# Kernel optimization log

Measured on AMD Instinct MI355X. Metric: run time of the kernel, lower is better.

The kernel has to match this reference:

```python
import jax, jax.numpy as jnp
import numpy as np

B, P, S, FX, FY, D, DFF = 8, 1, 2048, 16, 16, 512, 2048


def _ln(x, g, b, eps=1e-6):
    m = jnp.mean(x, axis=-1, keepdims=True)
    v = jnp.var(x, axis=-1, keepdims=True)
    return g * (x - m) / jnp.sqrt(v + eps) + b


def setup_inputs() -> dict:
    key = jax.random.key(0)
    ks = jax.random.split(key, 16)
    sc = 0.02
    inp = {
        'inputs': jax.random.normal(ks[0], (B, P, S, FX), dtype=jnp.float32),
        'targets': jax.random.normal(ks[1], (B, P, S, FY), dtype=jnp.float32),
        # input projection Dense(d_model)
        'Wp': jax.random.normal(ks[2], (FX, D), dtype=jnp.float32) * sc,
        'bp': jnp.zeros((D,), jnp.float32),
        # attention projections wq/wk/wv/dense (all Dense(d_model))
        'Wq': jax.random.normal(ks[3], (D, D), dtype=jnp.float32) * sc,
        'bq': jnp.zeros((D,), jnp.float32),
        'Wk': jax.random.normal(ks[4], (D, D), dtype=jnp.float32) * sc,
        'bk': jnp.zeros((D,), jnp.float32),
        'Wv': jax.random.normal(ks[5], (D, D), dtype=jnp.float32) * sc,
        'bv': jnp.zeros((D,), jnp.float32),
        'Wo': jax.random.normal(ks[6], (D, D), dtype=jnp.float32) * sc,
        'bo': jnp.zeros((D,), jnp.float32),
        # layernorm 1 / 2
        'g1': jnp.ones((D,), jnp.float32),
        'beta1': jnp.zeros((D,), jnp.float32),
        'g2': jnp.ones((D,), jnp.float32),
        'beta2': jnp.zeros((D,), jnp.float32),
        # pointwise FFN Dense(dff, relu) -> Dense(d_model)
        'Wf1': jax.random.normal(ks[7], (D, DFF), dtype=jnp.float32) * sc,
        'bf1': jnp.zeros((DFF,), jnp.float32),
        'Wf2': jax.random.normal(ks[8], (DFF, D), dtype=jnp.float32) * sc,
        'bf2': jnp.zeros((D,), jnp.float32),
        # final output layer Dense(output_size)
        'Wfin': jax.random.normal(ks[9], (D, FY), dtype=jnp.float32) * sc,
        'bfin': jnp.zeros((FY,), jnp.float32),
    }
    return inp


def reference(inputs, targets, Wp, bp, Wq, bq, Wk, bk, Wv, bv, Wo, bo,
              g1, beta1, g2, beta2, Wf1, bf1, Wf2, bf2, Wfin, bfin):
    d = jnp.float32(Wp.shape[1])
    # projection_layer_ts then *sqrt(d_model)
    x = (inputs @ Wp + bp) * jnp.sqrt(d)                      # (B,P,S,D)
    q = x @ Wq + bq
    k = x @ Wk + bk
    v = x @ Wv + bv
    # with noise=False and no resampling, the per-step SMC recurrence equals
    # causal self-attention (at step t, K/V hold rows <= t, rest are zero-masked)
    logits = jnp.einsum('bpqd,bpkd->bpqk', q, k) / jnp.sqrt(d)  # (B,P,S,S)
    Sdim = x.shape[2]
    causal = jnp.tril(jnp.ones((Sdim, Sdim), dtype=bool))
    logits = jnp.where(causal, logits, jnp.float32(-1e9))
    attn = jax.nn.softmax(logits, axis=-1)                    # attention weights per step
    z = jnp.einsum('bpqk,bpkd->bpqd', attn, v)
    z = z @ Wo + bo
    # full_model: LN(z+x) -> FFN -> LN(ffn+out)
    out = _ln(z + x, g1, beta1)
    ff = jax.nn.relu(out @ Wf1 + bf1) @ Wf2 + bf2
    r = _ln(ff + out, g2, beta2)                              # R trajectory (B,P,S,D)
    pred = r @ Wfin + bfin                                    # (B,P,S,F_y)
    # no resampling (noise=False): R_resampl == R, pred_resampl == pred
    return (pred, pred, k, v, r, attn)
```

## Files before the change

### kernel.cpp

```cpp
#include <hip/hip_runtime.h>
#include <hip/hip_bf16.h>
#include <stdint.h>

#define BB 8
#define SS 2048
#define TT (BB*SS)
#define DD 512
#define DFFX 2048

static __device__ const float SQRTD  = 22.627416997969522f;
static __device__ const float INVSQD = 0.04419417382415922f;

typedef __attribute__((ext_vector_type(4))) float  f32x4_t;
typedef __attribute__((ext_vector_type(8))) __bf16 bf16x8_t;
typedef __attribute__((ext_vector_type(4))) __bf16 bf16x4_t;
typedef __attribute__((ext_vector_type(2))) __bf16 bf16x2_t;

static __device__ __forceinline__ bf16x8_t mk_frag(bf16x4_t lo, bf16x4_t hi) {
  return __builtin_shufflevector(lo, hi, 0, 1, 2, 3, 4, 5, 6, 7);
}

typedef __attribute__((address_space(1))) const unsigned int g_u32;
typedef __attribute__((address_space(3))) unsigned int lds_u32;
static __device__ __forceinline__ void gld16(const void* g, void* l) {
  __builtin_amdgcn_global_load_lds((g_u32*)g, (lds_u32*)l, 16, 0, 0);
}

__global__ __launch_bounds__(256) void transpose_conv3(
    const float* __restrict__ Wo, const float* __restrict__ Wf1,
    const float* __restrict__ Wf2, __bf16* __restrict__ Wo_t,
    __bf16* __restrict__ Wf1_t, __bf16* __restrict__ Wf2_t) {
  const int bx = blockIdx.x;
  const float* src; __bf16* dst; int C, R, gx, gy;
  if (bx < 256)       { src = Wo;  dst = Wo_t;  R = 512;  C = 512;  gx = bx & 15;  gy = bx >> 4; }
  else if (bx < 1280) { const int b = bx - 256;  src = Wf1; dst = Wf1_t; R = 512;  C = 2048; gx = b & 63; gy = b >> 6; }
  else                { const int b = bx - 1280; src = Wf2; dst = Wf2_t; R = 2048; C = 512;  gx = b & 15; gy = b >> 4; }
  __shared__ float tile[32][33];
  const int c0 = gx * 32, r0 = gy * 32;
  const int tx = threadIdx.x & 31, ty = threadIdx.x >> 5;
#pragma unroll
  for (int i = 0; i < 4; i++)
    tile[ty + 8*i][tx] = src[(size_t)(r0 + ty + 8*i) * C + c0 + tx];
  __syncthreads();
#pragma unroll
  for (int i = 0; i < 4; i++)
    dst[(size_t)(c0 + ty + 8*i) * R + r0 + tx] = (__bf16)tile[tx][ty + 8*i];
}

__global__ __launch_bounds__(256) void fold_kernel(
    const float* __restrict__ Wp, const float* __restrict__ bp,
    const float* __restrict__ Wq, const float* __restrict__ bq,
    const float* __restrict__ Wk, const float* __restrict__ bk,
    const float* __restrict__ Wv, const float* __restrict__ bv,
    float* __restrict__ Wfold, float* __restrict__ bfold) {
  __shared__ float wp[16][512];
  __shared__ float bps[512];
  for (int i = threadIdx.x; i < 16 * 512; i += 256) wp[i >> 9][i & 511] = Wp[i];
  for (int i = threadIdx.x; i < 512; i += 256) bps[i] = bp[i];
  __syncthreads();
  const int cl = threadIdx.x & 15, r = threadIdx.x >> 4;
  const int cg = blockIdx.x * 16 + cl;
  const int sub = cg >> 9, wc = cg & 511;
  const float* W = sub == 0 ? Wq : sub == 1 ? Wk : Wv;
  const float* bb = sub == 0 ? bq : sub == 1 ? bk : bv;
  float acc = 0.f, bacc = 0.f;
  for (int k = 0; k < 512; k += 4) {
    const float4 wpv = *(const float4*)&wp[r][k];
    const float g0 = W[(size_t)k * 512 + wc];
    const float g1 = W[(size_t)(k + 1) * 512 + wc];
    const float g2 = W[(size_t)(k + 2) * 512 + wc];
    const float g3 = W[(size_t)(k + 3) * 512 + wc];
    acc += wpv.x * g0 + wpv.y * g1 + wpv.z * g2 + wpv.w * g3;
    if (r == 0) {
      const float4 b4 = *(const float4*)&bps[k];
      bacc += b4.x * g0 + b4.y * g1 + b4.z * g2 + b4.w * g3;
    }
  }
  Wfold[(size_t)r * 1536 + cg] = acc * SQRTD;
  if (r == 0) bfold[cg] = bacc * SQRTD + bb[wc];
}

__global__ __launch_bounds__(256) void smallk_kernel(
    const float* __restrict__ inp,
    const float* __restrict__ Wfold, const float* __restrict__ bfold,
    const float* __restrict__ Wp, const float* __restrict__ bp,
    __bf16* __restrict__ qb, __bf16* __restrict__ kb, __bf16* __restrict__ vb,
    __bf16* __restrict__ xb, float* __restrict__ o_k, float* __restrict__ o_v) {
  const int sl = blockIdx.y;
  const float* W; const float* bias; int ldw; float scale;
  __bf16* ob; float* fo;
  if (sl == 3) { W = Wp; bias = bp; ldw = 512; scale = SQRTD; ob = xb; fo = nullptr; }
  else {
    W = Wfold + sl * 512; bias = bfold + sl * 512; ldw = 1536; scale = 1.f;
    ob = sl == 0 ? qb : sl == 1 ? kb : vb;
    fo = sl == 0 ? (float*)nullptr : sl == 1 ? o_k : o_v;
  }
  __shared__ float ivl[16][16];
  const int tid = threadIdx.x;
  ivl[tid >> 4][tid & 15] = inp[(size_t)blockIdx.x * 256 + tid];
  const int c0 = 2 * tid;
  float w0[16], w1[16];
#pragma unroll
  for (int r = 0; r < 16; r++) {
    w0[r] = W[(size_t)r * ldw + c0];
    w1[r] = W[(size_t)r * ldw + c0 + 1];
  }
  const float bb0 = bias[c0], bb1 = bias[c0 + 1];
  __syncthreads();
#pragma unroll 4
  for (int tt = 0; tt < 16; ++tt) {
    const float4 i0 = *(const float4*)&ivl[tt][0];
    const float4 i1 = *(const float4*)&ivl[tt][4];
    const float4 i2 = *(const float4*)&ivl[tt][8];
    const float4 i3 = *(const float4*)&ivl[tt][12];
    float a0, a1;
    a0  = i0.x * w0[0];   a1  = i0.x * w1[0];
    a0 += i0.y * w0[1];   a1 += i0.y * w1[1];
    a0 += i0.z * w0[2];   a1 += i0.z * w1[2];
    a0 += i0.w * w0[3];   a1 += i0.w * w1[3];
    a0 += i1.x * w0[4];   a1 += i1.x * w1[4];
    a0 += i1.y * w0[5];   a1 += i1.y * w1[5];
    a0 += i1.z * w0[6];   a1 += i1.z * w1[6];
    a0 += i1.w * w0[7];   a1 += i1.w * w1[7];
    a0 += i2.x * w0[8];   a1 += i2.x * w1[8];
    a0 += i2.y * w0[9];   a1 += i2.y * w1[9];
    a0 += i2.z * w0[10];  a1 += i2.z * w1[10];
    a0 += i2.w * w0[11];  a1 += i2.w * w1[11];
    a0 += i3.x * w0[12];  a1 += i3.x * w1[12];
    a0 += i3.y * w0[13];  a1 += i3.y * w1[13];
    a0 += i3.z * w0[14];  a1 += i3.z * w1[14];
    a0 += i3.w * w0[15];  a1 += i3.w * w1[15];
    const float v0 = (a0 + bb0) * scale;
    const float v1 = (a1 + bb1) * scale;
    const size_t t = (size_t)blockIdx.x * 16 + tt;
    bf16x2_t pv; pv[0] = (__bf16)v0; pv[1] = (__bf16)v1;
    *(bf16x2_t*)(ob + t * 512 + c0) = pv;
    if (fo) {
      float2 fv; fv.x = v0; fv.y = v1;
      *(float2*)(fo + t * 512 + c0) = fv;
    }
  }
}

__global__ __launch_bounds__(256) void attn_prep_kernel(
    const __bf16* __restrict__ qbuf, const __bf16* __restrict__ kbuf,
    const __bf16* __restrict__ vbuf, const __bf16* __restrict__ Wo_t,
    __bf16* __restrict__ pb, __bf16* __restrict__ vwt) {
  const int bx = blockIdx.x, by = blockIdx.y;
  const int z = blockIdx.z;
  const int m0 = by * 128;
  const bool isScore = bx < 16;
  const int n0 = (isScore ? bx : bx - 16) * 128;
  if (isScore && n0 > m0 + 127) return;
  const __bf16* A  = (isScore ? qbuf : vbuf) + (size_t)z * SS * DD;
  const __bf16* Bt = isScore ? (kbuf + (size_t)z * SS * DD) : Wo_t;
  constexpr int K = DD;

  __shared__ __align__(16) __bf16 As[3 * 128 * 32];
  __shared__ __align__(16) __bf16 Bs[3 * 128 * 32];
  const int tid = threadIdx.x, lane = tid & 63, wave = tid >> 6;
  const int l15 = lane & 15, g = lane >> 4;
  const int wr = wave >> 1, wc = wave & 1;

  const int srow0 = wave * 32 + (lane >> 2);
  const int srow1 = srow0 + 16;
  const int sc0 = (((lane & 3) ^ ((srow0 >> 1) & 3)) << 4);
  const int sc1 = (((lane & 3) ^ ((srow1 >> 1) & 3)) << 4);
  const char* ga0 = (const char*)(A + (size_t)(m0 + srow0) * K) + sc0;
  const char* ga1 = (const char*)(A + (size_t)(m0 + srow1) * K) + sc1;
  const char* gb0 = (const char*)(Bt + (size_t)(n0 + srow0) * K) + sc0;
  const char* gb1 = (const char*)(Bt + (size_t)(n0 + srow1) * K) + sc1;

  const int plo = (g >> 1) ^ ((l15 >> 1) & 3);
  const int aof0 = (wr * 64 + l15) * 64 + plo * 16 + (g & 1) * 8;
  const int bof0 = (wc * 64 + l15) * 64 + plo * 16 + (g & 1) * 8;

  f32x4_t acc[4][4];
#pragma unroll
  for (int i = 0; i < 4; i++)
#pragma unroll
    for (int j = 0; j < 4; j++) acc[i][j] = (f32x4_t){0.f, 0.f, 0.f, 0.f};

  auto STAGE = [&](const int buf, const int k0) {
    const size_t kb = (size_t)k0 * 2;
    char* la = (char*)As + buf * 8192 + wave * 2048;
    char* lb = (char*)Bs + buf * 8192 + wave * 2048;
    gld16(ga0 + kb, la);
    gld16(ga1 + kb, la + 1024);
    gld16(gb0 + kb, lb);
    gld16(gb1 + kb, lb + 1024);
  };
  auto COMPUTE = [&](const int buf) {
    const char* AsB = (const char*)As + buf * 8192;
    const char* BsB = (const char*)Bs + buf * 8192;
    bf16x8_t af[4], bfr[4];
#pragma unroll
    for (int i = 0; i < 4; i++) {
      const int ao = aof0 + i * 1024;
      af[i] = mk_frag(*(const bf16x4_t*)(AsB + ao),
                      *(const bf16x4_t*)(AsB + (ao ^ 32)));
      const int bo = bof0 + i * 1024;
      bfr[i] = mk_frag(*(const bf16x4_t*)(BsB + bo),
                       *(const bf16x4_t*)(BsB + (bo ^ 32)));
    }
#pragma unroll
    for (int i = 0; i < 4; i++)
#pragma unroll
      for (int j = 0; j < 4; j++)
        acc[i][j] = __builtin_amdgcn_mfma_f32_16x16x32_bf16(af[i], bfr[j], acc[i][j], 0, 0, 0);
  };

  const int nt = K >> 5;
  STAGE(0, 0);
  STAGE(1, 32);
  STAGE(2, 64);
  int cur = 0;
  for (int t = 0; t < nt; ++t) {
    const int rem = nt - 1 - t;
    if (rem >= 2)      asm volatile("s_waitcnt vmcnt(8)" ::: "memory");
    else if (rem == 1) asm volatile("s_waitcnt vmcnt(4)" ::: "memory");
    else               asm volatile("s_waitcnt vmcnt(0)" ::: "memory");
    __builtin_amdgcn_s_barrier();
    COMPUTE(cur);
    __builtin_amdgcn_s_barrier();
    if (t + 3 < nt) STAGE(cur, (t + 3) << 5);
    cur = (cur == 2) ? 0 : cur + 1;
  }

#pragma unroll
  for (int i = 0; i < 4; i++) {
#pragma unroll
    for (int j = 0; j < 4; j++) {
      const int col = n0 + wc * 64 + j * 16 + l15;
      if (isScore) {
#pragma unroll
        for (int r = 0; r < 4; r++) {
          const int row = m0 + wr * 64 + i * 16 + g * 4 + r;
          pb[(size_t)z * SS * SS + (size_t)row * SS + col] =
              (__bf16)(acc[i][j][r] * INVSQD);
        }
      } else {
        const int row0 = m0 + wr * 64 + i * 16 + g * 4;
        bf16x4_t tv;
#pragma unroll
        for (int r = 0; r < 4; r++) tv[r] = (__bf16)acc[i][j][r];
        *(bf16x4_t*)(vwt + (size_t)z * SS * DD + (size_t)col * SS + row0) = tv;
      }
    }
  }
}

template <bool CAUSAL, bool RELU, bool RES, bool XCDS>
__global__ __launch_bounds__(256) void gemm128(
    const __bf16* __restrict__ A, const __bf16* __restrict__ Bt,
    const float* __restrict__ bias, const __bf16* __restrict__ Res,
    __bf16* __restrict__ Cb,
    int N, int K, size_t aBatch, size_t bBatch, size_t cBatch) {
  int bx = blockIdx.x, by = blockIdx.y;
  if (XCDS) {
    const int nwg = (int)(gridDim.x * gridDim.y);
    const int cpx = nwg >> 3;
    const int lin = (int)(blockIdx.y * gridDim.x + blockIdx.x);
    const int nl = (lin & 7) * cpx + (lin >> 3);
    by = nl / (int)gridDim.x;
    bx = nl - by * (int)gridDim.x;
  }
  const int n0 = bx * 128;
  const int m0 = by * 128;
  __shared__ __align__(16) __bf16 As[3 * 128 * 32];
  __shared__ __align__(16) __bf16 Bs[3 * 128 * 32];
  const int tid = threadIdx.x, lane = tid & 63, wave = tid >> 6;
  const int l15 = lane & 15, g = lane >> 4;
  const int wr = wave >> 1, wc = wave & 1;

  const int srow0 = wave * 32 + (lane >> 2);
  const int srow1 = srow0 + 16;
  const int sc0 = (((lane & 3) ^ ((srow0 >> 1) & 3)) << 4);
  const int sc1 = (((lane & 3) ^ ((srow1 >> 1) & 3)) << 4);
  const size_t aOff = (size_t)blockIdx.z * aBatch;
  const size_t bOff = (size_t)blockIdx.z * bBatch;
  const size_t cOff = (size_t)blockIdx.z * cBatch;
  const char* gb0 = (const char*)(Bt + bOff + (size_t)(n0 + srow0) * K) + sc0;
  const char* gb1 = (const char*)(Bt + bOff + (size_t)(n0 + srow1) * K) + sc1;
  const char* ga0 = (const char*)(A + aOff + (size_t)(m0 + srow0) * K) + sc0;
  const char* ga1 = (const char*)(A + aOff + (size_t)(m0 + srow1) * K) + sc1;

  const int plo = (g >> 1) ^ ((l15 >> 1) & 3);
  const int aof0 = (wr * 64 + l15) * 64 + plo * 16 + (g & 1) * 8;
  const int bof0 = (wc * 64 + l15) * 64 + plo * 16 + (g & 1) * 8;

  f32x4_t acc[4][4];
#pragma unroll
  for (int i = 0; i < 4; i++)
#pragma unroll
    for (int j = 0; j < 4; j++) acc[i][j] = (f32x4_t){0.f, 0.f, 0.f, 0.f};

  auto STAGE = [&](const int buf, const int k0) {
    const size_t kb = (size_t)k0 * 2;
    char* la = (char*)As + buf * 8192 + wave * 2048;
    char* lb = (char*)Bs + buf * 8192 + wave * 2048;
    gld16(ga0 + kb, la);
    gld16(ga1 + kb, la + 1024);
    gld16(gb0 + kb, lb);
    gld16(gb1 + kb, lb + 1024);
  };
  auto COMPUTE = [&](const int buf) {
    const char* AsB = (const char*)As + buf * 8192;
    const char* BsB = (const char*)Bs + buf * 8192;
    bf16x8_t af[4], bfr[4];
#pragma unroll
    for (int i = 0; i < 4; i++) {
      const int ao = aof0 + i * 1024;
      af[i] = mk_frag(*(const bf16x4_t*)(AsB + ao),
                      *(const bf16x4_t*)(AsB + (ao ^ 32)));
      const int bo = bof0 + i * 1024;
      bfr[i] = mk_frag(*(const bf16x4_t*)(BsB + bo),
                       *(const bf16x4_t*)(BsB + (bo ^ 32)));
    }
#pragma unroll
    for (int i = 0; i < 4; i++)
#pragma unroll
      for (int j = 0; j < 4; j++)
        acc[i][j] = __builtin_amdgcn_mfma_f32_16x16x32_bf16(af[i], bfr[j], acc[i][j], 0, 0, 0);
  };

  const int kend = CAUSAL ? (m0 + 128) : K;
  const int nt = kend >> 5;
  STAGE(0, 0);
  STAGE(1, 32);
  STAGE(2, 64);
  int cur = 0;
  for (int t = 0; t < nt; ++t) {
    const int rem = nt - 1 - t;
    if (rem >= 2)      asm volatile("s_waitcnt vmcnt(8)" ::: "memory");
    else if (rem == 1) asm volatile("s_waitcnt vmcnt(4)" ::: "memory");
    else               asm volatile("s_waitcnt vmcnt(0)" ::: "memory");
    __builtin_amdgcn_s_barrier();
    COMPUTE(cur);
    __builtin_amdgcn_s_barrier();
    if (t + 3 < nt) STAGE(cur, (t + 3) << 5);
    cur = (cur == 2) ? 0 : cur + 1;
  }

#pragma unroll
  for (int i = 0; i < 4; i++) {
#pragma unroll
    for (int j = 0; j < 4; j++) {
      const int col = n0 + wc * 64 + j * 16 + l15;
      const float bv = bias ? bias[col] : 0.f;
#pragma unroll
      for (int r = 0; r < 4; r++) {
        const int row = m0 + wr * 64 + i * 16 + g * 4 + r;
        float v = acc[i][j][r] + bv;
        if (RELU) v = fmaxf(v, 0.f);
        if (RES) v += (float)Res[cOff + (size_t)row * N + col];
        Cb[cOff + (size_t)row * N + col] = (__bf16)v;
      }
    }
  }
}

__global__ __launch_bounds__(256) void softmax_kernel(
    float* __restrict__ att, __bf16* __restrict__ pb) {
  const int t = blockIdx.x * 4 + (threadIdx.x >> 6);
  const int gq = t & (SS - 1);
  const int lane = threadIdx.x & 63;
  float* row = att + (size_t)t * SS;
  __bf16* prow = pb + (size_t)t * SS;
  const int nch = (gq >> 9) + 1;
  const int wlim = ((gq & ~127) + 128 + 511) >> 9;
  float x[32];
  float m = -1e30f;
#pragma unroll
  for (int ch = 0; ch < 4; ch++) {
    float* xp = &x[ch * 8];
    if (ch < nch) {
      const int c0 = ch * 512 + lane * 8;
      bf16x8_t v = *(const bf16x8_t*)(prow + c0);
#pragma unroll
      for (int j = 0; j < 8; j++) {
        const float f = (float)v[j];
        xp[j] = (c0 + j <= gq) ? f : -1e30f;
        m = fmaxf(m, xp[j]);
      }
    } else {
#pragma unroll
      for (int j = 0; j < 8; j++) xp[j] = -1e30f;
    }
  }
#pragma unroll
  for (int off = 1; off < 64; off <<= 1) m = fmaxf(m, __shfl_xor(m, off, 64));
  float s = 0.f;
#pragma unroll
  for (int i = 0; i < 32; i++) { x[i] = __expf(x[i] - m); s += x[i]; }
#pragma unroll
  for (int off = 1; off < 64; off <<= 1) s += __shfl_xor(s, off, 64);
  const float inv = 1.f / s;
#pragma unroll
  for (int ch = 0; ch < 4; ch++) {
    const int c0 = ch * 512 + lane * 8;
    float o[8];
    bf16x8_t ov;
#pragma unroll
    for (int j = 0; j < 8; j++) {
      const float pv = x[ch * 8 + j] * inv;
      o[j] = pv;
      ov[j] = (__bf16)pv;
    }
    float4 f0, f1;
    f0.x = o[0]; f0.y = o[1]; f0.z = o[2]; f0.w = o[3];
    f1.x = o[4]; f1.y = o[5]; f1.z = o[6]; f1.w = o[7];
    *(float4*)(row + c0) = f0;
    *(float4*)(row + c0 + 4) = f1;
    if (ch < wlim) *(bf16x8_t*)(prow + c0) = ov;
  }
}

__global__ __launch_bounds__(256) void ln_kernel(
    const __bf16* __restrict__ X, const float* __restrict__ gam,
    const float* __restrict__ bet, __bf16* __restrict__ Ob) {
  const int t = blockIdx.x * 4 + (threadIdx.x >> 6);
  const int lane = threadIdx.x & 63;
  const int d0 = lane * 8;
  bf16x8_t xv = *(const bf16x8_t*)(X + (size_t)t * DD + d0);
  float x[8];
#pragma unroll
  for (int j = 0; j < 8; j++) x[j] = (float)xv[j];
  float s = 0.f, sq = 0.f;
#pragma unroll
  for (int j = 0; j < 8; j++) { s += x[j]; sq += x[j] * x[j]; }
#pragma unroll
  for (int off = 1; off < 64; off <<= 1) {
    s += __shfl_xor(s, off, 64);
    sq += __shfl_xor(sq, off, 64);
  }
  const float mean = s * (1.f / 512.f);
  const float var = sq * (1.f / 512.f) - mean * mean;
  const float rstd = rsqrtf(var + 1e-6f);
  float4 g0 = *(const float4*)(gam + d0), g1v = *(const float4*)(gam + d0 + 4);
  float4 b0 = *(const float4*)(bet + d0), b1v = *(const float4*)(bet + d0 + 4);
  float gg[8] = {g0.x, g0.y, g0.z, g0.w, g1v.x, g1v.y, g1v.z, g1v.w};
  float bb2[8] = {b0.x, b0.y, b0.z, b0.w, b1v.x, b1v.y, b1v.z, b1v.w};
  bf16x8_t ov;
#pragma unroll
  for (int j = 0; j < 8; j++)
    ov[j] = (__bf16)((x[j] - mean) * rstd * gg[j] + bb2[j]);
  *(bf16x8_t*)(Ob + (size_t)t * DD + d0) = ov;
}

__global__ __launch_bounds__(256) void ln_final_kernel(
    const __bf16* __restrict__ X, const float* __restrict__ gam,
    const float* __restrict__ bet, float* __restrict__ Of,
    const float* __restrict__ Wfin, const float* __restrict__ bfin,
    float* __restrict__ P1, float* __restrict__ P2) {
  __shared__ float wfs[512][16];
  __shared__ float rf[4][516];
  for (int i = threadIdx.x; i < 512 * 16; i += 256) wfs[i >> 4][i & 15] = Wfin[i];
  const int tw = threadIdx.x >> 6;
  const int t = blockIdx.x * 4 + tw;
  const int lane = threadIdx.x & 63;
  const int d0 = lane * 8;
  bf16x8_t xv = *(const bf16x8_t*)(X + (size_t)t * DD + d0);
  float x[8];
#pragma unroll
  for (int j = 0; j < 8; j++) x[j] = (float)xv[j];
  float s = 0.f, sq = 0.f;
#pragma unroll
  for (int j = 0; j < 8; j++) { s += x[j]; sq += x[j] * x[j]; }
#pragma unroll
  for (int off = 1; off < 64; off <<= 1) {
    s += __shfl_xor(s, off, 64);
    sq += __shfl_xor(sq, off, 64);
  }
  const float mean = s * (1.f / 512.f);
  const float var = sq * (1.f / 512.f) - mean * mean;
  const float rstd = rsqrtf(var + 1e-6f);
  float4 g0 = *(const float4*)(gam + d0), g1v = *(const float4*)(gam + d0 + 4);
  float4 b0 = *(const float4*)(bet + d0), b1v = *(const float4*)(bet + d0 + 4);
  float gg[8] = {g0.x, g0.y, g0.z, g0.w, g1v.x, g1v.y, g1v.z, g1v.w};
  float bb2[8] = {b0.x, b0.y, b0.z, b0.w, b1v.x, b1v.y, b1v.z, b1v.w};
  float o[8];
  float4 f0, f1;
#pragma unroll
  for (int j = 0; j < 8; j++) {
    o[j] = (x[j] - mean) * rstd * gg[j] + bb2[j];
    rf[tw][d0 + j] = o[j];
  }
  f0.x = o[0]; f0.y = o[1]; f0.z = o[2]; f0.w = o[3];
  f1.x = o[4]; f1.y = o[5]; f1.z = o[6]; f1.w = o[7];
  *(float4*)(Of + (size_t)t * DD + d0) = f0;
  *(float4*)(Of + (size_t)t * DD + d0 + 4) = f1;
  __syncthreads();
  if (threadIdx.x < 64) {
    const int tt = threadIdx.x >> 4, n = threadIdx.x & 15;
    float acc = 0.f;
#pragma unroll 4
    for (int k = 0; k < 512; k += 4) {
      const float4 rv = *(const float4*)&rf[tt][k];
      acc += rv.x * wfs[k][n] + rv.y * wfs[k + 1][n] +
             rv.z * wfs[k + 2][n] + rv.w * wfs[k + 3][n];
    }
    const float v = acc + bfin[n];
    const size_t tok = (size_t)blockIdx.x * 4 + tt;
    P1[tok * 16 + n] = v;
    P2[tok * 16 + n] = v;
  }
}

extern "C" void kernel_launch(void* const* d_in, const int* in_sizes, int n_in,
                              void* d_out, int out_size, void* d_ws, size_t ws_size,
                              hipStream_t stream) {
  const float* inp  = (const float*)d_in[0];
  const float* Wp   = (const float*)d_in[2];
  const float* bp   = (const float*)d_in[3];
  const float* Wq   = (const float*)d_in[4];
  const float* bq   = (const float*)d_in[5];
  const float* Wk   = (const float*)d_in[6];
  const float* bk   = (const float*)d_in[7];
  const float* Wv   = (const float*)d_in[8];
  const float* bv   = (const float*)d_in[9];
  const float* Wo   = (const float*)d_in[10];
  const float* bo   = (const float*)d_in[11];
  const float* g1   = (const float*)d_in[12];
  const float* be1  = (const float*)d_in[13];
  const float* g2   = (const float*)d_in[14];
  const float* be2  = (const float*)d_in[15];
  const float* Wf1  = (const float*)d_in[16];
  const float* bf1  = (const float*)d_in[17];
  const float* Wf2  = (const float*)d_in[18];
  const float* bf2  = (const float*)d_in[19];
  const float* Wfin = (const float*)d_in[20];
  const float* bfin = (const float*)d_in[21];
  (void)in_sizes; (void)n_in; (void)out_size; (void)ws_size;

  float* out = (float*)d_out;
  float* o_pred1 = out;
  float* o_pred2 = out + 262144;
  float* o_k     = out + 524288;
  float* o_v     = out + 8912896;
  float* o_r     = out + 17301504;
  float* o_att   = out + 25690112;

  char* base = (char*)d_ws;
  size_t off = 0;
  auto takeB = [&](size_t bytes) -> char* {
    char* p = base + off;
    off += (bytes + 255) & ~(size_t)255;
    return p;
  };
  float*  Wfold = (float*)takeB((size_t)16 * 1536 * 4);
  float*  bfold = (float*)takeB((size_t)1536 * 4);
  __bf16* Wo_t  = (__bf16*)takeB((size_t)DD * DD * 2);
  __bf16* Wf1_t = (__bf16*)takeB((size_t)DD * DFFX * 2);
  __bf16* Wf2_t = (__bf16*)takeB((size_t)DD * DFFX * 2);
  __bf16* xb    = (__bf16*)takeB((size_t)TT * DD * 2);
  __bf16* qbuf  = (__bf16*)takeB((size_t)TT * DD * 2);
  __bf16* kbuf  = (__bf16*)takeB((size_t)TT * DD * 2);
  __bf16* vbuf  = (__bf16*)takeB((size_t)TT * DD * 2);
  __bf16* vwt   = (__bf16*)takeB((size_t)TT * DD * 2);
  __bf16* h1b   = (__bf16*)takeB((size_t)TT * DD * 2);
  __bf16* lninb = (__bf16*)takeB((size_t)TT * DD * 2);
  __bf16* ffb   = (__bf16*)takeB((size_t)TT * DFFX * 2);
  __bf16* pb    = ffb;

  transpose_conv3<<<dim3(2304), 256, 0, stream>>>(Wo, Wf1, Wf2, Wo_t, Wf1_t, Wf2_t);

  fold_kernel<<<dim3(96), 256, 0, stream>>>(Wp, bp, Wq, bq, Wk, bk, Wv, bv,
                                            Wfold, bfold);

  smallk_kernel<<<dim3(TT / 16, 4), 256, 0, stream>>>(
      inp, Wfold, bfold, Wp, bp, qbuf, kbuf, vbuf, xb, o_k, o_v);

  attn_prep_kernel<<<dim3(20, 16, BB), 256, 0, stream>>>(
      qbuf, kbuf, vbuf, Wo_t, pb, vwt);

  softmax_kernel<<<dim3(TT / 4), 256, 0, stream>>>(o_att, pb);

  gemm128<true, false, true, false><<<dim3(4, 16, BB), 256, 0, stream>>>(
      pb, vwt, bo, xb, lninb, DD, SS,
      (size_t)SS * SS, (size_t)DD * SS, (size_t)SS * DD);

  ln_kernel<<<dim3(TT / 4), 256, 0, stream>>>(lninb, g1, be1, h1b);

  gemm128<false, true, false, true><<<dim3(16, 128, 1), 256, 0, stream>>>(
      h1b, Wf1_t, bf1, nullptr, ffb, DFFX, DD, 0, 0, 0);
  gemm128<false, false, true, true><<<dim3(4, 128, 1), 256, 0, stream>>>(
      ffb, Wf2_t, bf2, h1b, lninb, DD, DFFX, 0, 0, 0);

  ln_final_kernel<<<dim3(TT / 4), 256, 0, stream>>>(
      lninb, g2, be2, o_r, Wfin, bfin, o_pred1, o_pred2);
}
```

Before: 426.6 us.

## Merge weight-prep kernels and restructure GEMM pipeline to one barrier per step

```diff
diff --git a/kernel.cpp b/kernel.cpp
--- a/kernel.cpp
+++ b/kernel.cpp
@@ -26,58 +26,59 @@
   __builtin_amdgcn_global_load_lds((g_u32*)g, (lds_u32*)l, 16, 0, 0);
 }
 
-__global__ __launch_bounds__(256) void transpose_conv3(
+__global__ __launch_bounds__(256) void prep_kernel(
     const float* __restrict__ Wo, const float* __restrict__ Wf1,
     const float* __restrict__ Wf2, __bf16* __restrict__ Wo_t,
-    __bf16* __restrict__ Wf1_t, __bf16* __restrict__ Wf2_t) {
-  const int bx = blockIdx.x;
-  const float* src; __bf16* dst; int C, R, gx, gy;
-  if (bx < 256)       { src = Wo;  dst = Wo_t;  R = 512;  C = 512;  gx = bx & 15;  gy = bx >> 4; }
-  else if (bx < 1280) { const int b = bx - 256;  src = Wf1; dst = Wf1_t; R = 512;  C = 2048; gx = b & 63; gy = b >> 6; }
-  else                { const int b = bx - 1280; src = Wf2; dst = Wf2_t; R = 2048; C = 512;  gx = b & 15; gy = b >> 4; }
-  __shared__ float tile[32][33];
-  const int c0 = gx * 32, r0 = gy * 32;
-  const int tx = threadIdx.x & 31, ty = threadIdx.x >> 5;
-#pragma unroll
-  for (int i = 0; i < 4; i++)
-    tile[ty + 8*i][tx] = src[(size_t)(r0 + ty + 8*i) * C + c0 + tx];
-  __syncthreads();
-#pragma unroll
-  for (int i = 0; i < 4; i++)
-    dst[(size_t)(c0 + ty + 8*i) * R + r0 + tx] = (__bf16)tile[tx][ty + 8*i];
-}
-
-__global__ __launch_bounds__(256) void fold_kernel(
+    __bf16* __restrict__ Wf1_t, __bf16* __restrict__ Wf2_t,
     const float* __restrict__ Wp, const float* __restrict__ bp,
     const float* __restrict__ Wq, const float* __restrict__ bq,
     const float* __restrict__ Wk, const float* __restrict__ bk,
     const float* __restrict__ Wv, const float* __restrict__ bv,
     float* __restrict__ Wfold, float* __restrict__ bfold) {
+  __shared__ float tile[32][33];
   __shared__ float wp[16][512];
   __shared__ float bps[512];
-  for (int i = threadIdx.x; i < 16 * 512; i += 256) wp[i >> 9][i & 511] = Wp[i];
-  for (int i = threadIdx.x; i < 512; i += 256) bps[i] = bp[i];
-  __syncthreads();
-  const int cl = threadIdx.x & 15, r = threadIdx.x >> 4;
-  const int cg = blockIdx.x * 16 + cl;
-  const int sub = cg >> 9, wc = cg & 511;
-  const float* W = sub == 0 ? Wq : sub == 1 ? Wk : Wv;
-  const float* bb = sub == 0 ? bq : sub == 1 ? bk : bv;
-  float acc = 0.f, bacc = 0.f;
-  for (int k = 0; k < 512; k += 4) {
-    const float4 wpv = *(const float4*)&wp[r][k];
-    const float g0 = W[(size_t)k * 512 + wc];
-    const float g1 = W[(size_t)(k + 1) * 512 + wc];
-    const float g2 = W[(size_t)(k + 2) * 512 + wc];
-    const float g3 = W[(size_t)(k + 3) * 512 + wc];
-    acc += wpv.x * g0 + wpv.y * g1 + wpv.z * g2 + wpv.w * g3;
-    if (r == 0) {
-      const float4 b4 = *(const float4*)&bps[k];
-      bacc += b4.x * g0 + b4.y * g1 + b4.z * g2 + b4.w * g3;
-    }
-  }
-  Wfold[(size_t)r * 1536 + cg] = acc * SQRTD;
-  if (r == 0) bfold[cg] = bacc * SQRTD + bb[wc];
+  const int bxx = blockIdx.x;
+  if (bxx < 2304) {
+    const float* src; __bf16* dst; int C, R, gx, gy;
+    if (bxx < 256)       { src = Wo;  dst = Wo_t;  R = 512;  C = 512;  gx = bxx & 15; gy = bxx >> 4; }
+    else if (bxx < 1280) { const int b = bxx - 256;  src = Wf1; dst = Wf1_t; R = 512;  C = 2048; gx = b & 63; gy = b >> 6; }
+    else                 { const int b = bxx - 1280; src = Wf2; dst = Wf2_t; R = 2048; C = 512;  gx = b & 15; gy = b >> 4; }
+    const int c0 = gx * 32, r0 = gy * 32;
+    const int tx = threadIdx.x & 31, ty = threadIdx.x >> 5;
+#pragma unroll
+    for (int i = 0; i < 4; i++)
+      tile[ty + 8*i][tx] = src[(size_t)(r0 + ty + 8*i) * C + c0 + tx];
+    __syncthreads();
+#pragma unroll
+    for (int i = 0; i < 4; i++)
+      dst[(size_t)(c0 + ty + 8*i) * R + r0 + tx] = (__bf16)tile[tx][ty + 8*i];
+  } else {
+    const int fb = bxx - 2304;
+    for (int i = threadIdx.x; i < 16 * 512; i += 256) wp[i >> 9][i & 511] = Wp[i];
+    for (int i = threadIdx.x; i < 512; i += 256) bps[i] = bp[i];
+    __syncthreads();
+    const int cl = threadIdx.x & 15, r = threadIdx.x >> 4;
+    const int cg = fb * 16 + cl;
+    const int sub = cg >> 9, wc = cg & 511;
+    const float* W = sub == 0 ? Wq : sub == 1 ? Wk : Wv;
+    const float* bb = sub == 0 ? bq : sub == 1 ? bk : bv;
+    float acc = 0.f, bacc = 0.f;
+    for (int k = 0; k < 512; k += 4) {
+      const float4 wpv = *(const float4*)&wp[r][k];
+      const float g0 = W[(size_t)k * 512 + wc];
+      const float g1 = W[(size_t)(k + 1) * 512 + wc];
+      const float g2 = W[(size_t)(k + 2) * 512 + wc];
+      const float g3 = W[(size_t)(k + 3) * 512 + wc];
+      acc += wpv.x * g0 + wpv.y * g1 + wpv.z * g2 + wpv.w * g3;
+      if (r == 0) {
+        const float4 b4 = *(const float4*)&bps[k];
+        bacc += b4.x * g0 + b4.y * g1 + b4.z * g2 + b4.w * g3;
+      }
+    }
+    Wfold[(size_t)r * 1536 + cg] = acc * SQRTD;
+    if (r == 0) bfold[cg] = bacc * SQRTD + bb[wc];
+  }
 }
 
 __global__ __launch_bounds__(256) void smallk_kernel(
@@ -213,17 +214,13 @@
   const int nt = K >> 5;
   STAGE(0, 0);
   STAGE(1, 32);
-  STAGE(2, 64);
   int cur = 0;
   for (int t = 0; t < nt; ++t) {
-    const int rem = nt - 1 - t;
-    if (rem >= 2)      asm volatile("s_waitcnt vmcnt(8)" ::: "memory");
-    else if (rem == 1) asm volatile("s_waitcnt vmcnt(4)" ::: "memory");
-    else               asm volatile("s_waitcnt vmcnt(0)" ::: "memory");
+    if (t + 1 < nt) asm volatile("s_waitcnt vmcnt(4)" ::: "memory");
+    else            asm volatile("s_waitcnt vmcnt(0)" ::: "memory");
     __builtin_amdgcn_s_barrier();
+    if (t + 2 < nt) STAGE((cur + 2) % 3, (t + 2) << 5);
     COMPUTE(cur);
-    __builtin_amdgcn_s_barrier();
-    if (t + 3 < nt) STAGE(cur, (t + 3) << 5);
     cur = (cur == 2) ? 0 : cur + 1;
   }
 
@@ -328,17 +325,13 @@
   const int nt = kend >> 5;
   STAGE(0, 0);
   STAGE(1, 32);
-  STAGE(2, 64);
   int cur = 0;
   for (int t = 0; t < nt; ++t) {
-    const int rem = nt - 1 - t;
-    if (rem >= 2)      asm volatile("s_waitcnt vmcnt(8)" ::: "memory");
-    else if (rem == 1) asm volatile("s_waitcnt vmcnt(4)" ::: "memory");
-    else               asm volatile("s_waitcnt vmcnt(0)" ::: "memory");
+    if (t + 1 < nt) asm volatile("s_waitcnt vmcnt(4)" ::: "memory");
+    else            asm volatile("s_waitcnt vmcnt(0)" ::: "memory");
     __builtin_amdgcn_s_barrier();
+    if (t + 2 < nt) STAGE((cur + 2) % 3, (t + 2) << 5);
     COMPUTE(cur);
-    __builtin_amdgcn_s_barrier();
-    if (t + 3 < nt) STAGE(cur, (t + 3) << 5);
     cur = (cur == 2) ? 0 : cur + 1;
   }
 
@@ -563,10 +556,9 @@
   __bf16* ffb   = (__bf16*)takeB((size_t)TT * DFFX * 2);
   __bf16* pb    = ffb;
 
-  transpose_conv3<<<dim3(2304), 256, 0, stream>>>(Wo, Wf1, Wf2, Wo_t, Wf1_t, Wf2_t);
-
-  fold_kernel<<<dim3(96), 256, 0, stream>>>(Wp, bp, Wq, bq, Wk, bk, Wv, bv,
-                                            Wfold, bfold);
+  prep_kernel<<<dim3(2400), 256, 0, stream>>>(
+      Wo, Wf1, Wf2, Wo_t, Wf1_t, Wf2_t,
+      Wp, bp, Wq, bq, Wk, bk, Wv, bv, Wfold, bfold);
 
   smallk_kernel<<<dim3(TT / 16, 4), 256, 0, stream>>>(
       inp, Wfold, bfold, Wp, bp, qbuf, kbuf, vbuf, xb, o_k, o_v);
```

Result: slower. 439.4 us (+3.0%).
